# Kernel tuning notes

Hardware: AMD Instinct MI355X
Metric: run time of the kernel (lower is better)

## Reference

```python
import jax, jax.numpy as jnp
import numpy as np

IN, OUT, E, R = 2048, 2048, 8, 8

def setup_inputs() -> dict:
    key = jax.random.key(0)
    ks = jax.random.split(key, 8)
    B, S = 4, 2048
    x = jax.random.normal(ks[0], (B, S, IN), dtype=jnp.float32)
    routing_weights = jax.random.uniform(ks[1], (B, E), dtype=jnp.float32)
    W = jax.random.normal(ks[2], (OUT, IN), dtype=jnp.float32) / np.sqrt(IN).astype(np.float32)
    b = jax.random.normal(ks[3], (OUT,), dtype=jnp.float32) * 0.01
    lora_A_s = jax.random.normal(ks[4], (IN, R), dtype=jnp.float32) / np.sqrt(IN).astype(np.float32)
    lora_B_s = jax.random.normal(ks[5], (R, OUT), dtype=jnp.float32) * 0.01
    lora_A_e = jax.random.normal(ks[6], (E, IN, R), dtype=jnp.float32) / np.sqrt(IN).astype(np.float32)
    lora_B_e = jax.random.normal(ks[7], (E, R, OUT), dtype=jnp.float32) * 0.01
    return {"x": x, "routing_weights": routing_weights, "W": W, "b": b,
            "lora_A_s": lora_A_s, "lora_B_s": lora_B_s,
            "lora_A_e": lora_A_e, "lora_B_e": lora_B_e}

def reference(x, routing_weights, W, b, lora_A_s, lora_B_s, lora_A_e, lora_B_e):
    # base linear: [B,S,IN] @ [IN,OUT] + [OUT]
    base_out = jnp.einsum('bsi,oi->bso', x, W) + b
    # shared low-rank path
    shared_out = (x @ lora_A_s) @ lora_B_s
    # all experts batched: t[b,s,e,r] = x @ A_e[e]; weighted reduce over experts
    t = jnp.einsum('bsi,eir->bser', x, lora_A_e)          # [B,S,E,R]
    expert_out = jnp.einsum('bser,ero,be->bso', t, lora_B_e, routing_weights)
    return base_out + shared_out + expert_out
```

## Files before the change

kernel.cpp:

```cpp
#include <hip/hip_runtime.h>
#include <hip/hip_bf16.h>

#define IN_DIM 2048
#define OUT_DIM 2048
#define NE 8
#define M_TOT 8192
#define RANK_PAD 128
#define K_EXT 2176
#define NKT 34

typedef short short8 __attribute__((ext_vector_type(8)));
typedef float floatx4 __attribute__((ext_vector_type(4)));
typedef unsigned short us;

__device__ __forceinline__ us f2bf(float f) {
    union { float f; unsigned u; } v; v.f = f;
    unsigned r = v.u + 0x7FFFu + ((v.u >> 16) & 1u);
    return (us)(r >> 16);
}

__device__ __forceinline__ void gld_lds16(const void* g, void* l) {
    __builtin_amdgcn_global_load_lds(
        (const __attribute__((address_space(1))) void*)g,
        (__attribute__((address_space(3))) void*)l, 16, 0, 0);
}


__device__ __forceinline__ void stage2(const us* src, char* lds) {
    gld_lds16(src, lds);
    gld_lds16(src + 128 * K_EXT, lds + 8192);
}

__device__ __forceinline__ void mfma_quad(floatx4 (&acc)[8][4], const short8 (&af)[4],
                                          const short8 (&bf)[4], int mq) {
#pragma unroll
    for (int i = 0; i < 4; ++i)
#pragma unroll
        for (int ni = 0; ni < 4; ++ni)
            acc[mq * 4 + i][ni] =
                __builtin_amdgcn_mfma_f32_16x16x32_bf16(af[i], bf[ni], acc[mq * 4 + i][ni], 0, 0, 0);
}

template <int SM, int VM0, int VM2, bool RD3>
__device__ __forceinline__ void ktile(
    const us* __restrict__ pA, const us* __restrict__ pB, int k1, int k2,
    const char* smC, const char* smN, char* lwC, char* lwN,
    int ab, int bb,
    short8 (&afA)[4], short8 (&afB)[4], short8 (&bfA)[4], short8 (&bfB)[4],
    floatx4 (&acc)[8][4])
{
#pragma unroll
    for (int i = 0; i < 4; ++i) afB[i] = *(const short8*)(smC + ab + (4 + i) * 1024);
    asm volatile("s_waitcnt lgkmcnt(4)" ::: "memory");
    __builtin_amdgcn_sched_barrier(0);
    __builtin_amdgcn_s_setprio(1);
    mfma_quad(acc, afA, bfA, 0);
    __builtin_amdgcn_s_setprio(0);
    if (SM & 1) stage2(pA + k1 + 32, lwN + 32768);
    if (VM0 == 8)      asm volatile("s_waitcnt vmcnt(8)" ::: "memory");
    else if (VM0 == 0) asm volatile("s_waitcnt vmcnt(0)" ::: "memory");
    __builtin_amdgcn_s_barrier();

#pragma unroll
    for (int i = 0; i < 4; ++i) afA[i] = *(const short8*)(smC + 32768 + ab + (4 + i) * 1024);
#pragma unroll
    for (int i = 0; i < 4; ++i) bfB[i] = *(const short8*)(smC + 32768 + bb + i * 1024);
    asm volatile("s_waitcnt lgkmcnt(8)" ::: "memory");
    __builtin_amdgcn_sched_barrier(0);
    __builtin_amdgcn_s_setprio(1);
    mfma_quad(acc, afB, bfA, 1);
    __builtin_amdgcn_s_setprio(0);
    if (SM & 2) stage2(pB + k2, lwC + 16384);
    __builtin_amdgcn_s_barrier();

#pragma unroll
    for (int i = 0; i < 4; ++i) afB[i] = *(const short8*)(smC + 32768 + ab + i * 1024);
    asm volatile("s_waitcnt lgkmcnt(4)" ::: "memory");
    __builtin_amdgcn_sched_barrier(0);
    __builtin_amdgcn_s_setprio(1);
    mfma_quad(acc, afA, bfB, 1);
    __builtin_amdgcn_s_setprio(0);
    if (SM & 4) stage2(pA + k2, lwC);
    if (VM2 == 8)      asm volatile("s_waitcnt vmcnt(8)" ::: "memory");
    else if (VM2 == 4) asm volatile("s_waitcnt vmcnt(4)" ::: "memory");
    __builtin_amdgcn_s_barrier();

    if (RD3) {
#pragma unroll
        for (int i = 0; i < 4; ++i) afA[i] = *(const short8*)(smN + ab + i * 1024);
#pragma unroll
        for (int i = 0; i < 4; ++i) bfA[i] = *(const short8*)(smN + bb + i * 1024);
        asm volatile("s_waitcnt lgkmcnt(8)" ::: "memory");
    } else {
        asm volatile("s_waitcnt lgkmcnt(0)" ::: "memory");
    }
    __builtin_amdgcn_sched_barrier(0);
    __builtin_amdgcn_s_setprio(1);
    mfma_quad(acc, afB, bfB, 0);
    __builtin_amdgcn_s_setprio(0);
    if (SM & 8) stage2(pB + k2 + 32, lwC + 49152);
    __builtin_amdgcn_s_barrier();
}

__global__ __launch_bounds__(512) void main_gemm8(const us* __restrict__ A,
                                                  const us* __restrict__ B,
                                                  const float* __restrict__ bias,
                                                  float* __restrict__ out) {
    extern __shared__ char smem[];
    int tid = threadIdx.x;
    int lane = tid & 63, w = tid >> 6;
    int wm = w >> 2, wn = w & 3;
    int rlo = lane & 15, kq = lane >> 4;

    int b = blockIdx.x;
    int bs = (b & 7) * 32 + (b >> 3);
    int m0 = (bs >> 3) * 256, n0 = (bs & 7) * 256;

    int swz = (kq ^ ((rlo >> 1) & 3)) * 16;
    int ab = (wm * 128 + rlo) * 64 + swz;
    int bb = 16384 + (wn * 64 + rlo) * 64 + swz;

    int r0 = tid >> 2;
    int ps = tid & 3;
    int ssw = (ps ^ ((r0 >> 1) & 3)) * 8;
    const us* pA = A + (size_t)(m0 + r0) * K_EXT + ssw;
    const us* pB = B + (size_t)(n0 + r0) * K_EXT + ssw;
    char* lw0 = smem + w * 1024;
    char* lw1 = lw0 + 65536;
    const char* sm0 = smem;
    const char* sm1 = smem + 65536;

    floatx4 acc[8][4];
#pragma unroll
    for (int mi = 0; mi < 8; ++mi)
#pragma unroll
        for (int ni = 0; ni < 4; ++ni) acc[mi][ni] = (floatx4)0.f;

    stage2(pA,      lw0);
    stage2(pB,      lw0 + 16384);
    stage2(pA + 32, lw0 + 32768);
    stage2(pB + 32, lw0 + 49152);
    stage2(pA + 64, lw1);
    stage2(pB + 64, lw1 + 16384);
    stage2(pB + 96, lw1 + 49152);
    asm volatile("s_waitcnt vmcnt(10)" ::: "memory");
    __builtin_amdgcn_s_barrier();

    short8 afA[4], afB[4], bfA[4], bfB[4];
#pragma unroll
    for (int i = 0; i < 4; ++i) afA[i] = *(const short8*)(sm0 + ab + i * 1024);
#pragma unroll
    for (int i = 0; i < 4; ++i) bfA[i] = *(const short8*)(sm0 + bb + i * 1024);

    for (int tt = 0; tt < 16; ++tt) {
        int t0 = tt * 2;
        ktile<0xF, 8, 8, true>(pA, pB, (t0 + 1) * 64, (t0 + 2) * 64,
                               sm0, sm1, lw0, lw1, ab, bb, afA, afB, bfA, bfB, acc);
        ktile<0xF, 8, 8, true>(pA, pB, (t0 + 2) * 64, (t0 + 3) * 64,
                               sm1, sm0, lw1, lw0, ab, bb, afA, afB, bfA, bfB, acc);
    }
    ktile<0x1, 8, 4, true>(pA, pB, 33 * 64, 34 * 64,
                           sm0, sm1, lw0, lw1, ab, bb, afA, afB, bfA, bfB, acc);
    ktile<0x0, 0, -1, false>(pA, pB, 0, 0,
                             sm1, sm0, lw1, lw0, ab, bb, afA, afB, bfA, bfB, acc);

    float bbias[4];
#pragma unroll
    for (int ni = 0; ni < 4; ++ni) bbias[ni] = bias[n0 + wn * 64 + ni * 16 + rlo];
#pragma unroll
    for (int mi = 0; mi < 8; ++mi) {
        int row = m0 + wm * 128 + mi * 16 + kq * 4;
#pragma unroll
        for (int ni = 0; ni < 4; ++ni) {
            int col = n0 + wn * 64 + ni * 16 + rlo;
#pragma unroll
            for (int r = 0; r < 4; ++r)
                out[(size_t)(row + r) * OUT_DIM + col] = acc[mi][ni][r] + bbias[ni];
        }
    }
}

__global__ void prep_w(const float* __restrict__ W, const float* __restrict__ Bs,
                       const float* __restrict__ Be, us* __restrict__ Bext) {
    int n = blockIdx.x;
    int t = threadIdx.x;
    const float4* src = (const float4*)(W + (size_t)n * IN_DIM + t * 8);
    float4 v0 = src[0], v1 = src[1];
    short8 o;
    o[0] = (short)f2bf(v0.x); o[1] = (short)f2bf(v0.y); o[2] = (short)f2bf(v0.z); o[3] = (short)f2bf(v0.w);
    o[4] = (short)f2bf(v1.x); o[5] = (short)f2bf(v1.y); o[6] = (short)f2bf(v1.z); o[7] = (short)f2bf(v1.w);
    *(short8*)(Bext + (size_t)n * K_EXT + t * 8) = o;
    if (t < RANK_PAD) {
        float v = 0.f;
        if (t < 8)       v = Bs[(size_t)t * OUT_DIM + n];
        else if (t < 72) v = Be[(size_t)(t - 8) * OUT_DIM + n];
        Bext[(size_t)n * K_EXT + IN_DIM + t] = f2bf(v);
    }
}

__global__ void prep_acat(const float* __restrict__ As, const float* __restrict__ Ae,
                          us* __restrict__ AcatT) {
    int kp = blockIdx.x;
    int i0 = threadIdx.x * 8;
    short8 o;
#pragma unroll
    for (int j = 0; j < 8; ++j) {
        int i = i0 + j;
        float v = 0.f;
        if (kp < 8)       v = As[(size_t)i * 8 + kp];
        else if (kp < 72) v = Ae[(size_t)((kp - 8) >> 3) * IN_DIM * 8 + (size_t)i * 8 + ((kp - 8) & 7)];
        o[j] = (short)f2bf(v);
    }
    *(short8*)(AcatT + (size_t)kp * IN_DIM + i0) = o;
}

__global__ __launch_bounds__(256) void tgemm_fused(const float* __restrict__ x,
                                                   us* __restrict__ Aext,
                                                   const us* __restrict__ AcatT,
                                                   const float* __restrict__ routing) {
    __shared__ floatx4 red[4][64][6];
    int tid = threadIdx.x;
    int lane = tid & 63, w = tid >> 6;
    int rlo = lane & 15, kq = lane >> 4;
    int mbase = blockIdx.x * 16;

    floatx4 acc[6];
#pragma unroll
    for (int ni = 0; ni < 6; ++ni) acc[ni] = (floatx4)0.f;

    const float* xrow = x + (size_t)(mbase + rlo) * IN_DIM + w * 512 + kq * 8;
    us* arow = Aext + (size_t)(mbase + rlo) * K_EXT + w * 512 + kq * 8;
    const us* bbase = AcatT + (size_t)rlo * IN_DIM + w * 512 + kq * 8;

#pragma unroll 4
    for (int kt = 0; kt < 16; ++kt) {
        int k0 = kt * 32;
        float4 v0 = *(const float4*)(xrow + k0);
        float4 v1 = *(const float4*)(xrow + k0 + 4);
        short8 a;
        a[0] = (short)f2bf(v0.x); a[1] = (short)f2bf(v0.y); a[2] = (short)f2bf(v0.z); a[3] = (short)f2bf(v0.w);
        a[4] = (short)f2bf(v1.x); a[5] = (short)f2bf(v1.y); a[6] = (short)f2bf(v1.z); a[7] = (short)f2bf(v1.w);
        *(short8*)(arow + k0) = a;
#pragma unroll
        for (int ni = 0; ni < 6; ++ni) {
            short8 bfr = *(const short8*)(bbase + (size_t)(ni * 16) * IN_DIM + k0);
            acc[ni] = __builtin_amdgcn_mfma_f32_16x16x32_bf16(a, bfr, acc[ni], 0, 0, 0);
        }
    }

#pragma unroll
    for (int ni = 0; ni < 6; ++ni) red[w][lane][ni] = acc[ni];
    __syncthreads();
    if (w == 0) {
#pragma unroll
        for (int ni = 0; ni < 6; ++ni) {
            floatx4 s = red[0][lane][ni];
#pragma unroll
            for (int ww = 1; ww < 4; ++ww) s += red[ww][lane][ni];
            int col = ni * 16 + rlo;
#pragma unroll
            for (int r = 0; r < 4; ++r) {
                int row = mbase + kq * 4 + r;
                float fac = (col < 8) ? 1.f
                          : (col < 72 ? routing[(row >> 11) * NE + ((col - 8) >> 3)] : 0.f);
                Aext[(size_t)row * K_EXT + IN_DIM + col] = f2bf(s[r] * fac);
            }
        }
#pragma unroll
        for (int c = 0; c < 2; ++c) {
            int col = 96 + c * 16 + rlo;
#pragma unroll
            for (int r = 0; r < 4; ++r)
                Aext[(size_t)(mbase + kq * 4 + r) * K_EXT + IN_DIM + col] = 0;
        }
    }
}

extern "C" void kernel_launch(void* const* d_in, const int* in_sizes, int n_in,
                              void* d_out, int out_size, void* d_ws, size_t ws_size,
                              hipStream_t stream) {
    const float* x   = (const float*)d_in[0];
    const float* rw  = (const float*)d_in[1];
    const float* W   = (const float*)d_in[2];
    const float* bv  = (const float*)d_in[3];
    const float* As  = (const float*)d_in[4];
    const float* Bs  = (const float*)d_in[5];
    const float* Ae  = (const float*)d_in[6];
    const float* Be  = (const float*)d_in[7];
    float* out = (float*)d_out;

    size_t offA = 0;
    size_t offB = offA + (size_t)M_TOT * K_EXT * sizeof(us);
    size_t offC = offB + (size_t)OUT_DIM * K_EXT * sizeof(us);
    size_t need = offC + (size_t)96 * IN_DIM * sizeof(us);
    if (ws_size < need) return;

    us* Aext  = (us*)((char*)d_ws + offA);
    us* Bext  = (us*)((char*)d_ws + offB);
    us* AcatT = (us*)((char*)d_ws + offC);

    hipFuncSetAttribute((const void*)main_gemm8,
                        hipFuncAttributeMaxDynamicSharedMemorySize, 131072);

    prep_acat<<<96, 256, 0, stream>>>(As, Ae, AcatT);
    prep_w<<<OUT_DIM, 256, 0, stream>>>(W, Bs, Be, Bext);
    tgemm_fused<<<M_TOT / 16, 256, 0, stream>>>(x, Aext, AcatT, rw);
    main_gemm8<<<256, 512, 131072, stream>>>(Aext, Bext, bv, out);
}
```

Before: 117.4 us.

## Switch main GEMM to 32x32x16 MFMA and merge prep kernels

```diff
diff --git a/kernel.cpp b/kernel.cpp
--- a/kernel.cpp
+++ b/kernel.cpp
@@ -11,12 +11,12 @@
 
 typedef short short8 __attribute__((ext_vector_type(8)));
 typedef float floatx4 __attribute__((ext_vector_type(4)));
+typedef float floatx16 __attribute__((ext_vector_type(16)));
 typedef unsigned short us;
 
 __device__ __forceinline__ us f2bf(float f) {
-    union { float f; unsigned u; } v; v.f = f;
-    unsigned r = v.u + 0x7FFFu + ((v.u >> 16) & 1u);
-    return (us)(r >> 16);
+    __hip_bfloat16 h = __float2bfloat16(f);
+    return *reinterpret_cast<us*>(&h);
 }
 
 __device__ __forceinline__ void gld_lds16(const void* g, void* l) {
@@ -31,54 +31,70 @@
     gld_lds16(src + 128 * K_EXT, lds + 8192);
 }
 
-__device__ __forceinline__ void mfma_quad(floatx4 (&acc)[8][4], const short8 (&af)[4],
-                                          const short8 (&bf)[4], int mq) {
-#pragma unroll
-    for (int i = 0; i < 4; ++i)
-#pragma unroll
-        for (int ni = 0; ni < 4; ++ni)
-            acc[mq * 4 + i][ni] =
-                __builtin_amdgcn_mfma_f32_16x16x32_bf16(af[i], bf[ni], acc[mq * 4 + i][ni], 0, 0, 0);
+__device__ __forceinline__ void rd_af(short8 (&d)[4], const char* sm, int kh, int mq,
+                                      int ab, int so0, int so1) {
+    const char* p = sm + kh * 32768 + ab + mq * 4096;
+    d[0] = *(const short8*)(p + so0);
+    d[1] = *(const short8*)(p + so1);
+    d[2] = *(const short8*)(p + 2048 + so0);
+    d[3] = *(const short8*)(p + 2048 + so1);
+}
+
+__device__ __forceinline__ void rd_bf(short8 (&d)[4], const char* sm, int kh,
+                                      int bb, int so0, int so1) {
+    const char* p = sm + kh * 32768 + bb;
+    d[0] = *(const short8*)(p + so0);
+    d[1] = *(const short8*)(p + so1);
+    d[2] = *(const short8*)(p + 2048 + so0);
+    d[3] = *(const short8*)(p + 2048 + so1);
+}
+
+__device__ __forceinline__ void mfma_oct(floatx16 (&acc)[4][2], const short8 (&af)[4],
+                                         const short8 (&bf)[4], int mq) {
+#pragma unroll
+    for (int ks = 0; ks < 2; ++ks)
+#pragma unroll
+        for (int ml = 0; ml < 2; ++ml)
+#pragma unroll
+            for (int nj = 0; nj < 2; ++nj)
+                acc[mq * 2 + ml][nj] = __builtin_amdgcn_mfma_f32_32x32x16_bf16(
+                    af[ml * 2 + ks], bf[nj * 2 + ks], acc[mq * 2 + ml][nj], 0, 0, 0);
 }
 
 template <int SM, int VM0, int VM2, bool RD3>
 __device__ __forceinline__ void ktile(
     const us* __restrict__ pA, const us* __restrict__ pB, int k1, int k2,
     const char* smC, const char* smN, char* lwC, char* lwN,
-    int ab, int bb,
+    int ab, int bb, int so0, int so1,
     short8 (&afA)[4], short8 (&afB)[4], short8 (&bfA)[4], short8 (&bfB)[4],
-    floatx4 (&acc)[8][4])
+    floatx16 (&acc)[4][2])
 {
-#pragma unroll
-    for (int i = 0; i < 4; ++i) afB[i] = *(const short8*)(smC + ab + (4 + i) * 1024);
+    rd_af(afB, smC, 0, 1, ab, so0, so1);
     asm volatile("s_waitcnt lgkmcnt(4)" ::: "memory");
     __builtin_amdgcn_sched_barrier(0);
     __builtin_amdgcn_s_setprio(1);
-    mfma_quad(acc, afA, bfA, 0);
+    mfma_oct(acc, afA, bfA, 0);
     __builtin_amdgcn_s_setprio(0);
     if (SM & 1) stage2(pA + k1 + 32, lwN + 32768);
     if (VM0 == 8)      asm volatile("s_waitcnt vmcnt(8)" ::: "memory");
     else if (VM0 == 0) asm volatile("s_waitcnt vmcnt(0)" ::: "memory");
     __builtin_amdgcn_s_barrier();
 
-#pragma unroll
-    for (int i = 0; i < 4; ++i) afA[i] = *(const short8*)(smC + 32768 + ab + (4 + i) * 1024);
-#pragma unroll
-    for (int i = 0; i < 4; ++i) bfB[i] = *(const short8*)(smC + 32768 + bb + i * 1024);
+    rd_af(afA, smC, 1, 1, ab, so0, so1);
+    rd_bf(bfB, smC, 1, bb, so0, so1);
     asm volatile("s_waitcnt lgkmcnt(8)" ::: "memory");
     __builtin_amdgcn_sched_barrier(0);
     __builtin_amdgcn_s_setprio(1);
-    mfma_quad(acc, afB, bfA, 1);
+    mfma_oct(acc, afB, bfA, 1);
     __builtin_amdgcn_s_setprio(0);
     if (SM & 2) stage2(pB + k2, lwC + 16384);
     __builtin_amdgcn_s_barrier();
 
-#pragma unroll
-    for (int i = 0; i < 4; ++i) afB[i] = *(const short8*)(smC + 32768 + ab + i * 1024);
+    rd_af(afB, smC, 1, 0, ab, so0, so1);
     asm volatile("s_waitcnt lgkmcnt(4)" ::: "memory");
     __builtin_amdgcn_sched_barrier(0);
     __builtin_amdgcn_s_setprio(1);
-    mfma_quad(acc, afA, bfB, 1);
+    mfma_oct(acc, afA, bfB, 1);
     __builtin_amdgcn_s_setprio(0);
     if (SM & 4) stage2(pA + k2, lwC);
     if (VM2 == 8)      asm volatile("s_waitcnt vmcnt(8)" ::: "memory");
@@ -86,17 +102,15 @@
     __builtin_amdgcn_s_barrier();
 
     if (RD3) {
-#pragma unroll
-        for (int i = 0; i < 4; ++i) afA[i] = *(const short8*)(smN + ab + i * 1024);
-#pragma unroll
-        for (int i = 0; i < 4; ++i) bfA[i] = *(const short8*)(smN + bb + i * 1024);
+        rd_af(afA, smN, 0, 0, ab, so0, so1);
+        rd_bf(bfA, smN, 0, bb, so0, so1);
         asm volatile("s_waitcnt lgkmcnt(8)" ::: "memory");
     } else {
         asm volatile("s_waitcnt lgkmcnt(0)" ::: "memory");
     }
     __builtin_amdgcn_sched_barrier(0);
     __builtin_amdgcn_s_setprio(1);
-    mfma_quad(acc, afB, bfB, 0);
+    mfma_oct(acc, afB, bfB, 0);
     __builtin_amdgcn_s_setprio(0);
     if (SM & 8) stage2(pB + k2 + 32, lwC + 49152);
     __builtin_amdgcn_s_barrier();
@@ -110,15 +124,17 @@
     int tid = threadIdx.x;
     int lane = tid & 63, w = tid >> 6;
     int wm = w >> 2, wn = w & 3;
-    int rlo = lane & 15, kq = lane >> 4;
+    int rl = lane & 31, hi = lane >> 5;
+    int swl = (rl >> 1) & 3;
 
     int b = blockIdx.x;
     int bs = (b & 7) * 32 + (b >> 3);
     int m0 = (bs >> 3) * 256, n0 = (bs & 7) * 256;
 
-    int swz = (kq ^ ((rlo >> 1) & 3)) * 16;
-    int ab = (wm * 128 + rlo) * 64 + swz;
-    int bb = 16384 + (wn * 64 + rlo) * 64 + swz;
+    int ab = (wm * 128 + rl) * 64;
+    int bb = 16384 + (wn * 64 + rl) * 64;
+    int so0 = (hi ^ swl) * 16;
+    int so1 = ((2 + hi) ^ swl) * 16;
 
     int r0 = tid >> 2;
     int ps = tid & 3;
@@ -130,11 +146,11 @@
     const char* sm0 = smem;
     const char* sm1 = smem + 65536;
 
-    floatx4 acc[8][4];
-#pragma unroll
-    for (int mi = 0; mi < 8; ++mi)
-#pragma unroll
-        for (int ni = 0; ni < 4; ++ni) acc[mi][ni] = (floatx4)0.f;
+    floatx16 acc[4][2];
+#pragma unroll
+    for (int mi = 0; mi < 4; ++mi)
+#pragma unroll
+        for (int nj = 0; nj < 2; ++nj) acc[mi][nj] = (floatx16)0.f;
 
     stage2(pA,      lw0);
     stage2(pB,      lw0 + 16384);
@@ -147,71 +163,76 @@
     __builtin_amdgcn_s_barrier();
 
     short8 afA[4], afB[4], bfA[4], bfB[4];
-#pragma unroll
-    for (int i = 0; i < 4; ++i) afA[i] = *(const short8*)(sm0 + ab + i * 1024);
-#pragma unroll
-    for (int i = 0; i < 4; ++i) bfA[i] = *(const short8*)(sm0 + bb + i * 1024);
+    rd_af(afA, sm0, 0, 0, ab, so0, so1);
+    rd_bf(bfA, sm0, 0, bb, so0, so1);
 
     for (int tt = 0; tt < 16; ++tt) {
         int t0 = tt * 2;
         ktile<0xF, 8, 8, true>(pA, pB, (t0 + 1) * 64, (t0 + 2) * 64,
-                               sm0, sm1, lw0, lw1, ab, bb, afA, afB, bfA, bfB, acc);
+                               sm0, sm1, lw0, lw1, ab, bb, so0, so1,
+                               afA, afB, bfA, bfB, acc);
         ktile<0xF, 8, 8, true>(pA, pB, (t0 + 2) * 64, (t0 + 3) * 64,
-                               sm1, sm0, lw1, lw0, ab, bb, afA, afB, bfA, bfB, acc);
+                               sm1, sm0, lw1, lw0, ab, bb, so0, so1,
+                               afA, afB, bfA, bfB, acc);
     }
     ktile<0x1, 8, 4, true>(pA, pB, 33 * 64, 34 * 64,
-                           sm0, sm1, lw0, lw1, ab, bb, afA, afB, bfA, bfB, acc);
+                           sm0, sm1, lw0, lw1, ab, bb, so0, so1,
+                           afA, afB, bfA, bfB, acc);
     ktile<0x0, 0, -1, false>(pA, pB, 0, 0,
-                             sm1, sm0, lw1, lw0, ab, bb, afA, afB, bfA, bfB, acc);
-
-    float bbias[4];
-#pragma unroll
-    for (int ni = 0; ni < 4; ++ni) bbias[ni] = bias[n0 + wn * 64 + ni * 16 + rlo];
-#pragma unroll
-    for (int mi = 0; mi < 8; ++mi) {
-        int row = m0 + wm * 128 + mi * 16 + kq * 4;
-#pragma unroll
-        for (int ni = 0; ni < 4; ++ni) {
-            int col = n0 + wn * 64 + ni * 16 + rlo;
-#pragma unroll
-            for (int r = 0; r < 4; ++r)
-                out[(size_t)(row + r) * OUT_DIM + col] = acc[mi][ni][r] + bbias[ni];
-        }
-    }
-}
-
-__global__ void prep_w(const float* __restrict__ W, const float* __restrict__ Bs,
-                       const float* __restrict__ Be, us* __restrict__ Bext) {
-    int n = blockIdx.x;
+                             sm1, sm0, lw1, lw0, ab, bb, so0, so1,
+                             afA, afB, bfA, bfB, acc);
+
+    float bb2[2];
+#pragma unroll
+    for (int nj = 0; nj < 2; ++nj) bb2[nj] = bias[n0 + wn * 64 + nj * 32 + rl];
+#pragma unroll
+    for (int mi = 0; mi < 4; ++mi) {
+#pragma unroll
+        for (int nj = 0; nj < 2; ++nj) {
+            int col = n0 + wn * 64 + nj * 32 + rl;
+#pragma unroll
+            for (int reg = 0; reg < 16; ++reg) {
+                int row = m0 + wm * 128 + mi * 32 + (reg & 3) + 8 * (reg >> 2) + 4 * hi;
+                out[(size_t)row * OUT_DIM + col] = acc[mi][nj][reg] + bb2[nj];
+            }
+        }
+    }
+}
+
+__global__ void prep_wb(const float* __restrict__ W, const float* __restrict__ Bs,
+                        const float* __restrict__ Be, const float* __restrict__ As,
+                        const float* __restrict__ Ae, us* __restrict__ Bext,
+                        us* __restrict__ AcatT) {
+    int blk = blockIdx.x;
     int t = threadIdx.x;
-    const float4* src = (const float4*)(W + (size_t)n * IN_DIM + t * 8);
-    float4 v0 = src[0], v1 = src[1];
-    short8 o;
-    o[0] = (short)f2bf(v0.x); o[1] = (short)f2bf(v0.y); o[2] = (short)f2bf(v0.z); o[3] = (short)f2bf(v0.w);
-    o[4] = (short)f2bf(v1.x); o[5] = (short)f2bf(v1.y); o[6] = (short)f2bf(v1.z); o[7] = (short)f2bf(v1.w);
-    *(short8*)(Bext + (size_t)n * K_EXT + t * 8) = o;
-    if (t < RANK_PAD) {
-        float v = 0.f;
-        if (t < 8)       v = Bs[(size_t)t * OUT_DIM + n];
-        else if (t < 72) v = Be[(size_t)(t - 8) * OUT_DIM + n];
-        Bext[(size_t)n * K_EXT + IN_DIM + t] = f2bf(v);
-    }
-}
-
-__global__ void prep_acat(const float* __restrict__ As, const float* __restrict__ Ae,
-                          us* __restrict__ AcatT) {
-    int kp = blockIdx.x;
-    int i0 = threadIdx.x * 8;
-    short8 o;
-#pragma unroll
-    for (int j = 0; j < 8; ++j) {
-        int i = i0 + j;
-        float v = 0.f;
-        if (kp < 8)       v = As[(size_t)i * 8 + kp];
-        else if (kp < 72) v = Ae[(size_t)((kp - 8) >> 3) * IN_DIM * 8 + (size_t)i * 8 + ((kp - 8) & 7)];
-        o[j] = (short)f2bf(v);
-    }
-    *(short8*)(AcatT + (size_t)kp * IN_DIM + i0) = o;
+    if (blk < OUT_DIM) {
+        int n = blk;
+        const float4* src = (const float4*)(W + (size_t)n * IN_DIM + t * 8);
+        float4 v0 = src[0], v1 = src[1];
+        short8 o;
+        o[0] = (short)f2bf(v0.x); o[1] = (short)f2bf(v0.y); o[2] = (short)f2bf(v0.z); o[3] = (short)f2bf(v0.w);
+        o[4] = (short)f2bf(v1.x); o[5] = (short)f2bf(v1.y); o[6] = (short)f2bf(v1.z); o[7] = (short)f2bf(v1.w);
+        *(short8*)(Bext + (size_t)n * K_EXT + t * 8) = o;
+        if (t < RANK_PAD) {
+            float v = 0.f;
+            if (t < 8)       v = Bs[(size_t)t * OUT_DIM + n];
+            else if (t < 72) v = Be[(size_t)(t - 8) * OUT_DIM + n];
+            Bext[(size_t)n * K_EXT + IN_DIM + t] = f2bf(v);
+        }
+    } else {
+        int kp = blk - OUT_DIM;
+        int i0 = t * 8;
+        short8 o;
+#pragma unroll
+        for (int j = 0; j < 8; ++j) {
+            int i = i0 + j;
+            float v = 0.f;
+            if (kp < 8)       v = As[(size_t)i * 8 + kp];
+            else if (kp < 72) v = Ae[(size_t)((kp - 8) >> 3) * IN_DIM * 8 + (size_t)i * 8 + ((kp - 8) & 7)];
+            o[j] = (short)f2bf(v);
+        }
+        *(short8*)(AcatT + (size_t)kp * IN_DIM + i0) = o;
+    }
 }
 
 __global__ __launch_bounds__(256) void tgemm_fused(const float* __restrict__ x,
@@ -302,8 +323,7 @@
     hipFuncSetAttribute((const void*)main_gemm8,
                         hipFuncAttributeMaxDynamicSharedMemorySize, 131072);
 
-    prep_acat<<<96, 256, 0, stream>>>(As, Ae, AcatT);
-    prep_w<<<OUT_DIM, 256, 0, stream>>>(W, Bs, Be, Bext);
+    prep_wb<<<OUT_DIM + 96, 256, 0, stream>>>(W, Bs, Be, As, Ae, Bext, AcatT);
     tgemm_fused<<<M_TOT / 16, 256, 0, stream>>>(x, Aext, AcatT, rw);
     main_gemm8<<<256, 512, 131072, stream>>>(Aext, Bext, bv, out);
 }
```

New measurement: 121.0 us. +3.1%, slower.
